# Optimization experiments

Measured on AMD Instinct MI355X. Metric: run time of the kernel, lower is better.

Reference implementation:

```python
import jax, jax.numpy as jnp
import numpy as np

N_NODES = 50000
N_EDGES = 800000
D_IN = 512
LATENT = [512, 512, 512]
L2_EPS = 1e-12  # torch F.normalize clamp_min


def _gin_layer(x, src, dst, W, b, eps):
    # sum aggregation of neighbor (source) features into destination nodes
    agg = jax.ops.segment_sum(x[src], dst, num_segments=x.shape[0])  # [N, d]
    h = agg + (1.0 + eps) * x
    return jax.nn.relu(h @ W + b)  # Sequential(Linear, ReLU)


def _l2_normalize(x):
    n = jnp.sqrt(jnp.sum(x * x, axis=-1, keepdims=True))
    return x / jnp.maximum(n, L2_EPS)


def setup_inputs() -> dict:
    key = jax.random.key(0)
    ks = jax.random.split(key, 10)
    x = jax.random.normal(ks[0], (N_NODES, D_IN), dtype=jnp.float32)
    edge_index = jax.random.randint(ks[1], (2, N_EDGES), 0, N_NODES, dtype=jnp.int32)
    dims = [D_IN] + LATENT
    inp = {"x": x, "edge_index": edge_index}
    for i in range(3):
        fan_in = dims[i]
        bound = 1.0 / np.sqrt(fan_in)
        inp[f"W{i+1}"] = jax.random.uniform(ks[2 + 2 * i], (dims[i], dims[i + 1]), jnp.float32, -bound, bound)
        inp[f"b{i+1}"] = jax.random.uniform(ks[3 + 2 * i], (dims[i + 1],), jnp.float32, -bound, bound)
        inp[f"eps{i+1}"] = jnp.zeros((), dtype=jnp.float32)  # train_eps=True, init 0
    return inp


def reference(x, edge_index, W1, b1, eps1, W2, b2, eps2, W3, b3, eps3):
    src, dst = edge_index[0], edge_index[1]
    # layers 0..num_layers-2: GINConv -> L2 normalize -> ReLU
    h = _gin_layer(x, src, dst, W1, b1, eps1)
    h = jax.nn.relu(_l2_normalize(h))
    h = _gin_layer(h, src, dst, W2, b2, eps2)
    h = jax.nn.relu(_l2_normalize(h))
    # final layer: raw GINConv output = logits
    logits = _gin_layer(h, src, dst, W3, b3, eps3)
    probs = jax.nn.softmax(logits, axis=-1)
    return (logits, probs)
```

## Files before the change

kernel.cpp:

```cpp
#include <hip/hip_runtime.h>
#include <stdint.h>

#define N_NODES 50000
#define N_EDGES 800000

typedef unsigned int uint32;

__device__ inline float bflo(uint32 u) { return __builtin_bit_cast(float, u << 16); }
__device__ inline float bfhi(uint32 u) { return __builtin_bit_cast(float, u & 0xffff0000u); }
__device__ inline float bf2f(unsigned short h) { return __builtin_bit_cast(float, (uint32)h << 16); }
__device__ inline unsigned short f2bf(float f) {
    uint32 u = __builtin_bit_cast(uint32, f);
    u += 0x7fffu + ((u >> 16) & 1u);
    return (unsigned short)(u >> 16);
}
__device__ inline uint32 pack2(float lo, float hi) {
    return (uint32)f2bf(lo) | ((uint32)f2bf(hi) << 16);
}

__global__ __launch_bounds__(256) void zero_k(int* p, int n) {
    int i = blockIdx.x * 256 + threadIdx.x;
    if (i < n) p[i] = 0;
}

__global__ __launch_bounds__(256) void count_k(const int* __restrict__ ei, int* __restrict__ cnt) {
    int e = blockIdx.x * 256 + threadIdx.x;
    if (e < N_EDGES) atomicAdd(&cnt[ei[N_EDGES + e]], 1);
}

#define NB 196

__global__ __launch_bounds__(256) void blocksum_k(const int* __restrict__ cnt, int* __restrict__ bsum) {
    int i = blockIdx.x * 256 + threadIdx.x;
    int v = (i < N_NODES) ? cnt[i] : 0;
#pragma unroll
    for (int off = 32; off > 0; off >>= 1) v += __shfl_down(v, off);
    __shared__ int sh[4];
    int w = threadIdx.x >> 6, lane = threadIdx.x & 63;
    if (lane == 0) sh[w] = v;
    __syncthreads();
    if (threadIdx.x == 0) bsum[blockIdx.x] = sh[0] + sh[1] + sh[2] + sh[3];
}

__global__ __launch_bounds__(256) void bscan_k(const int* __restrict__ bsum, int* __restrict__ bpre,
                                               int* __restrict__ rowptr) {
    __shared__ int sh[256];
    int t = threadIdx.x;
    int v = (t < NB) ? bsum[t] : 0;
    sh[t] = v;
    __syncthreads();
    for (int d = 1; d < 256; d <<= 1) {
        int u = (t >= d) ? sh[t - d] : 0;
        __syncthreads();
        sh[t] += u;
        __syncthreads();
    }
    if (t < NB) bpre[t] = sh[t] - v;
    if (t == NB - 1) rowptr[N_NODES] = sh[t];
}

__global__ __launch_bounds__(256) void scatter_k(int* __restrict__ cnt, const int* __restrict__ bpre,
                                                 int* __restrict__ rowptr) {
    int b = blockIdx.x, t = threadIdx.x, i = b * 256 + t;
    int w = t >> 6, lane = t & 63;
    int myv = (i < N_NODES) ? cnt[i] : 0;
    int v = myv;
#pragma unroll
    for (int d = 1; d < 64; d <<= 1) {
        int u = __shfl_up(v, d);
        if (lane >= d) v += u;
    }
    __shared__ int wt[4];
    if (lane == 63) wt[w] = v;
    __syncthreads();
    int off = bpre[b];
    for (int k = 0; k < w; k++) off += wt[k];
    int excl = v - myv + off;
    if (i < N_NODES) {
        rowptr[i] = excl;
        cnt[i] = excl;
    }
}

__global__ __launch_bounds__(256) void fill_k(const int* __restrict__ ei, int* __restrict__ cursor,
                                              int* __restrict__ csr) {
    int e = blockIdx.x * 256 + threadIdx.x;
    if (e < N_EDGES) {
        int d = ei[N_EDGES + e];
        int p = atomicAdd(&cursor[d], 1);
        csr[p] = ei[e];
    }
}

__global__ __launch_bounds__(256) void wprep_k(const float* __restrict__ W,
                                               unsigned short* __restrict__ Whi,
                                               unsigned short* __restrict__ Wlo) {
    __shared__ float sh[64][65];
    int bk = (blockIdx.x & 7) * 64;
    int bn = (blockIdx.x >> 3) * 64;
    int t = threadIdx.x;
    int lr = t >> 4;
    int lc4 = (t & 15) * 4;
#pragma unroll
    for (int i = 0; i < 4; i++) {
        int k = lr + i * 16;
        float4 v = *(const float4*)&W[(size_t)(bk + k) * 512 + bn + lc4];
        sh[k][lc4] = v.x; sh[k][lc4 + 1] = v.y; sh[k][lc4 + 2] = v.z; sh[k][lc4 + 3] = v.w;
    }
    __syncthreads();
#pragma unroll
    for (int i = 0; i < 4; i++) {
        int n = lr + i * 16;
        float w0 = sh[lc4][n], w1 = sh[lc4 + 1][n], w2 = sh[lc4 + 2][n], w3 = sh[lc4 + 3][n];
        ushort4 h, l;
        h.x = f2bf(w0); l.x = f2bf(w0 - bf2f(h.x));
        h.y = f2bf(w1); l.y = f2bf(w1 - bf2f(h.y));
        h.z = f2bf(w2); l.z = f2bf(w2 - bf2f(h.z));
        h.w = f2bf(w3); l.w = f2bf(w3 - bf2f(h.w));
        *(ushort4*)&Whi[(size_t)(bn + n) * 512 + bk + lc4] = h;
        *(ushort4*)&Wlo[(size_t)(bn + n) * 512 + bk + lc4] = l;
    }
}

__global__ __launch_bounds__(256) void xconv_k(const float4* __restrict__ x, uint2* __restrict__ xb) {
    int i = blockIdx.x * 256 + threadIdx.x;
    float4 v = x[i];
    uint2 o;
    o.x = pack2(v.x, v.y);
    o.y = pack2(v.z, v.w);
    xb[i] = o;
}

__global__ __launch_bounds__(256) void invn_k(const float* __restrict__ ss, float* __restrict__ invn) {
    int i = blockIdx.x * 256 + threadIdx.x;
    if (i < N_NODES) invn[i] = 1.0f / fmaxf(sqrtf(ss[i]), 1e-12f);
}

template <bool SCALED>
__global__ __launch_bounds__(256) void agg_k(const uint4* __restrict__ xin,
                                             const int* __restrict__ rowptr,
                                             const int* __restrict__ csr,
                                             const float* __restrict__ eps,
                                             const float* __restrict__ invn,
                                             uint4* __restrict__ hout) {
    int node = blockIdx.x * 4 + (threadIdx.x >> 6);
    int lane = threadIdx.x & 63;
    int beg = rowptr[node], end = rowptr[node + 1];
    float a0 = 0.f, a1 = 0.f, a2 = 0.f, a3 = 0.f, a4 = 0.f, a5 = 0.f, a6 = 0.f, a7 = 0.f;
    int e = beg;
    for (; e + 4 <= end; e += 4) {
        int s0 = csr[e], s1 = csr[e + 1], s2 = csr[e + 2], s3 = csr[e + 3];
        uint4 q0 = xin[(size_t)s0 * 64 + lane];
        uint4 q1 = xin[(size_t)s1 * 64 + lane];
        uint4 q2 = xin[(size_t)s2 * 64 + lane];
        uint4 q3 = xin[(size_t)s3 * 64 + lane];
        float w0 = SCALED ? invn[s0] : 1.0f;
        float w1 = SCALED ? invn[s1] : 1.0f;
        float w2 = SCALED ? invn[s2] : 1.0f;
        float w3 = SCALED ? invn[s3] : 1.0f;
        a0 = fmaf(w0, bflo(q0.x), fmaf(w1, bflo(q1.x), fmaf(w2, bflo(q2.x), fmaf(w3, bflo(q3.x), a0))));
        a1 = fmaf(w0, bfhi(q0.x), fmaf(w1, bfhi(q1.x), fmaf(w2, bfhi(q2.x), fmaf(w3, bfhi(q3.x), a1))));
        a2 = fmaf(w0, bflo(q0.y), fmaf(w1, bflo(q1.y), fmaf(w2, bflo(q2.y), fmaf(w3, bflo(q3.y), a2))));
        a3 = fmaf(w0, bfhi(q0.y), fmaf(w1, bfhi(q1.y), fmaf(w2, bfhi(q2.y), fmaf(w3, bfhi(q3.y), a3))));
        a4 = fmaf(w0, bflo(q0.z), fmaf(w1, bflo(q1.z), fmaf(w2, bflo(q2.z), fmaf(w3, bflo(q3.z), a4))));
        a5 = fmaf(w0, bfhi(q0.z), fmaf(w1, bfhi(q1.z), fmaf(w2, bfhi(q2.z), fmaf(w3, bfhi(q3.z), a5))));
        a6 = fmaf(w0, bflo(q0.w), fmaf(w1, bflo(q1.w), fmaf(w2, bflo(q2.w), fmaf(w3, bflo(q3.w), a6))));
        a7 = fmaf(w0, bfhi(q0.w), fmaf(w1, bfhi(q1.w), fmaf(w2, bfhi(q2.w), fmaf(w3, bfhi(q3.w), a7))));
    }
    for (; e < end; ++e) {
        int s0 = csr[e];
        uint4 q0 = xin[(size_t)s0 * 64 + lane];
        float w0 = SCALED ? invn[s0] : 1.0f;
        a0 = fmaf(w0, bflo(q0.x), a0); a1 = fmaf(w0, bfhi(q0.x), a1);
        a2 = fmaf(w0, bflo(q0.y), a2); a3 = fmaf(w0, bfhi(q0.y), a3);
        a4 = fmaf(w0, bflo(q0.z), a4); a5 = fmaf(w0, bfhi(q0.z), a5);
        a6 = fmaf(w0, bflo(q0.w), a6); a7 = fmaf(w0, bfhi(q0.w), a7);
    }
    uint4 qs = xin[(size_t)node * 64 + lane];
    float ws = (1.0f + eps[0]) * (SCALED ? invn[node] : 1.0f);
    a0 = fmaf(ws, bflo(qs.x), a0); a1 = fmaf(ws, bfhi(qs.x), a1);
    a2 = fmaf(ws, bflo(qs.y), a2); a3 = fmaf(ws, bfhi(qs.y), a3);
    a4 = fmaf(ws, bflo(qs.z), a4); a5 = fmaf(ws, bfhi(qs.z), a5);
    a6 = fmaf(ws, bflo(qs.w), a6); a7 = fmaf(ws, bfhi(qs.w), a7);
    uint4 o;
    o.x = pack2(a0, a1);
    o.y = pack2(a2, a3);
    o.z = pack2(a4, a5);
    o.w = pack2(a6, a7);
    hout[(size_t)node * 64 + lane] = o;
}

typedef __bf16 bf16x8 __attribute__((ext_vector_type(8)));
typedef float f32x4 __attribute__((ext_vector_type(4)));

__device__ inline void async16(const void* g, void* l) {
    __builtin_amdgcn_global_load_lds((const __attribute__((address_space(1))) void*)g,
                                     (__attribute__((address_space(3))) void*)l, 16, 0, 0);
}

template <bool SPLIT, bool F32OUT, bool NORM>
__global__ __launch_bounds__(256) void gemm_k(const unsigned short* __restrict__ A,
                                              const unsigned short* __restrict__ Whi,
                                              const unsigned short* __restrict__ Wlo,
                                              const float* __restrict__ bias,
                                              unsigned short* __restrict__ outB,
                                              float* __restrict__ outF,
                                              float* __restrict__ ssOut, int M) {
    constexpr int K = 512, N = 512, BK = 32, TM = 128;
    __shared__ unsigned short lds_a[TM * BK];
    __shared__ unsigned short lds_bh[TM * BK];
    __shared__ unsigned short lds_bl[SPLIT ? TM * BK : 16];
    const int t = threadIdx.x;
    const int w = t >> 6, lane = t & 63;
    const int wrow = w >> 1, wcol = w & 1;
    const int m0 = blockIdx.y * TM;
    const int n0 = blockIdx.x * TM;

    int r0 = w * 16 + (lane >> 2), cc = (lane & 3) * 8;
    int r1 = 64 + r0;
    int am0 = m0 + r0; am0 = am0 < M ? am0 : M - 1;
    int am1 = m0 + r1; am1 = am1 < M ? am1 : M - 1;
    const unsigned short* ag0 = A + (size_t)am0 * K + cc;
    const unsigned short* ag1 = A + (size_t)am1 * K + cc;
    const unsigned short* bh0 = Whi + (size_t)(n0 + r0) * K + cc;
    const unsigned short* bh1 = Whi + (size_t)(n0 + r1) * K + cc;
    const unsigned short* bl0 = Wlo + (size_t)(n0 + r0) * K + cc;
    const unsigned short* bl1 = Wlo + (size_t)(n0 + r1) * K + cc;
    unsigned short* la0 = lds_a + w * 512;
    unsigned short* la1 = lds_a + 2048 + w * 512;
    unsigned short* lh0 = lds_bh + w * 512;
    unsigned short* lh1 = lds_bh + 2048 + w * 512;
    unsigned short* ll0 = lds_bl + w * 512;
    unsigned short* ll1 = lds_bl + 2048 + w * 512;

    f32x4 acc[4][4] = {};
    const int quad = lane >> 4, l15 = lane & 15;
    const int arow = wrow * 64 + l15;
    const int brow = wcol * 64 + l15;

    for (int k0 = 0; k0 < K; k0 += BK) {
        __syncthreads();
        async16(ag0 + k0, la0);
        async16(ag1 + k0, la1);
        async16(bh0 + k0, lh0);
        async16(bh1 + k0, lh1);
        if (SPLIT) {
            async16(bl0 + k0, ll0);
            async16(bl1 + k0, ll1);
        }
        __syncthreads();
        bf16x8 af[4], bh[4], bl[4];
#pragma unroll
        for (int i = 0; i < 4; i++)
            af[i] = *(const bf16x8*)&lds_a[(arow + i * 16) * BK + quad * 8];
#pragma unroll
        for (int j = 0; j < 4; j++)
            bh[j] = *(const bf16x8*)&lds_bh[(brow + j * 16) * BK + quad * 8];
        if (SPLIT) {
#pragma unroll
            for (int j = 0; j < 4; j++)
                bl[j] = *(const bf16x8*)&lds_bl[(brow + j * 16) * BK + quad * 8];
        }
#pragma unroll
        for (int i = 0; i < 4; i++)
#pragma unroll
            for (int j = 0; j < 4; j++) {
                acc[i][j] = __builtin_amdgcn_mfma_f32_16x16x32_bf16(af[i], bh[j], acc[i][j], 0, 0, 0);
                if (SPLIT)
                    acc[i][j] = __builtin_amdgcn_mfma_f32_16x16x32_bf16(af[i], bl[j], acc[i][j], 0, 0, 0);
            }
    }

#pragma unroll
    for (int i = 0; i < 4; i++) {
        int mbase = m0 + wrow * 64 + i * 16 + quad * 4;
        float rs[4] = {0.f, 0.f, 0.f, 0.f};
#pragma unroll
        for (int j = 0; j < 4; j++) {
            int n = n0 + wcol * 64 + j * 16 + l15;
            float bv = bias[n];
#pragma unroll
            for (int r = 0; r < 4; r++) {
                int m = mbase + r;
                if (m < M) {
                    float v = fmaxf(acc[i][j][r] + bv, 0.0f);
                    if (NORM) rs[r] += v * v;
                    if (F32OUT) outF[(size_t)m * N + n] = v;
                    else        outB[(size_t)m * N + n] = f2bf(v);
                }
            }
        }
        if (NORM) {
#pragma unroll
            for (int r = 0; r < 4; r++) {
                float s = rs[r];
                s += __shfl_xor(s, 1);
                s += __shfl_xor(s, 2);
                s += __shfl_xor(s, 4);
                s += __shfl_xor(s, 8);
                int m = mbase + r;
                if (l15 == 0 && m < M) atomicAdd(&ssOut[m], s);
            }
        }
    }
}

__global__ __launch_bounds__(256) void softmax_k(const float* __restrict__ logits,
                                                 float* __restrict__ probs) {
    int node = blockIdx.x * 4 + (threadIdx.x >> 6);
    int lane = threadIdx.x & 63;
    const float4* zp = (const float4*)(logits + (size_t)node * 512);
    float4 q0 = zp[lane * 2], q1 = zp[lane * 2 + 1];
    float f[8] = {q0.x, q0.y, q0.z, q0.w, q1.x, q1.y, q1.z, q1.w};
    float m = f[0];
#pragma unroll
    for (int i = 1; i < 8; i++) m = fmaxf(m, f[i]);
#pragma unroll
    for (int off = 32; off > 0; off >>= 1) m = fmaxf(m, __shfl_xor(m, off));
    float e[8], s = 0.f;
#pragma unroll
    for (int i = 0; i < 8; i++) { e[i] = __expf(f[i] - m); s += e[i]; }
#pragma unroll
    for (int off = 32; off > 0; off >>= 1) s += __shfl_xor(s, off);
    float inv = 1.0f / s;
    float4* pp = (float4*)(probs + (size_t)node * 512);
    pp[lane * 2]     = make_float4(e[0] * inv, e[1] * inv, e[2] * inv, e[3] * inv);
    pp[lane * 2 + 1] = make_float4(e[4] * inv, e[5] * inv, e[6] * inv, e[7] * inv);
}

extern "C" void kernel_launch(void* const* d_in, const int* in_sizes, int n_in,
                              void* d_out, int out_size, void* d_ws, size_t ws_size,
                              hipStream_t stream) {
    (void)in_sizes; (void)n_in; (void)out_size; (void)ws_size;
    const float* x = (const float*)d_in[0];
    const int* ei = (const int*)d_in[1];
    const float* W1 = (const float*)d_in[2];
    const float* b1 = (const float*)d_in[3];
    const float* e1 = (const float*)d_in[4];
    const float* W2 = (const float*)d_in[5];
    const float* b2 = (const float*)d_in[6];
    const float* e2 = (const float*)d_in[7];
    const float* W3 = (const float*)d_in[8];
    const float* b3 = (const float*)d_in[9];
    const float* e3 = (const float*)d_in[10];
    float* out = (float*)d_out;
    float* out_logits = out;
    float* out_probs = out + (size_t)N_NODES * 512;

    char* ws = (char*)d_ws;
    int* rowptr = (int*)ws;
    int* cursor = rowptr + 50048;
    int* csr = cursor + 50048;
    float* invn = (float*)(csr + N_EDGES);
    int* bsum = (int*)(invn + 50048);
    int* bpre = bsum + 256;
    float* ss = (float*)(bpre + 256);
    float* ss1 = ss;
    float* ss2 = ss + 50048;
    unsigned short* Wsp = (unsigned short*)(ss + 2 * 50048);
    unsigned short* featA = Wsp + 3 * 524288;
    unsigned short* featB = featA + (size_t)N_NODES * 512;

    zero_k<<<196, 256, 0, stream>>>(cursor, N_NODES);
    zero_k<<<392, 256, 0, stream>>>((int*)ss, 2 * 50048);
    count_k<<<(N_EDGES + 255) / 256, 256, 0, stream>>>(ei, cursor);
    blocksum_k<<<NB, 256, 0, stream>>>(cursor, bsum);
    bscan_k<<<1, 256, 0, stream>>>(bsum, bpre, rowptr);
    scatter_k<<<NB, 256, 0, stream>>>(cursor, bpre, rowptr);
    fill_k<<<(N_EDGES + 255) / 256, 256, 0, stream>>>(ei, cursor, csr);

    wprep_k<<<64, 256, 0, stream>>>(W1, Wsp,           Wsp + 262144);
    wprep_k<<<64, 256, 0, stream>>>(W2, Wsp + 524288,  Wsp + 786432);
    wprep_k<<<64, 256, 0, stream>>>(W3, Wsp + 1048576, Wsp + 1310720);

    xconv_k<<<25000, 256, 0, stream>>>((const float4*)x, (uint2*)featB);

    dim3 ggrid(4, (N_NODES + 127) / 128);

    agg_k<false><<<12500, 256, 0, stream>>>((const uint4*)featB, rowptr, csr, e1, nullptr, (uint4*)featA);
    gemm_k<false, false, true><<<ggrid, 256, 0, stream>>>(featA, Wsp, Wsp + 262144, b1, featB, nullptr, ss1, N_NODES);
    invn_k<<<196, 256, 0, stream>>>(ss1, invn);
    agg_k<true><<<12500, 256, 0, stream>>>((const uint4*)featB, rowptr, csr, e2, invn, (uint4*)featA);
    gemm_k<false, false, true><<<ggrid, 256, 0, stream>>>(featA, Wsp + 524288, Wsp + 786432, b2, featB, nullptr, ss2, N_NODES);
    invn_k<<<196, 256, 0, stream>>>(ss2, invn);
    agg_k<true><<<12500, 256, 0, stream>>>((const uint4*)featB, rowptr, csr, e3, invn, (uint4*)featA);
    gemm_k<true, true, false><<<ggrid, 256, 0, stream>>>(featA, Wsp + 1048576, Wsp + 1310720, b3, nullptr, out_logits, nullptr, N_NODES);
    softmax_k<<<N_NODES / 4, 256, 0, stream>>>(out_logits, out_probs);
}
```

Measured before the change: 998.4 us.

## Fuse neighbor aggregation with GEMM, keeping aggregated tile in LDS

Merges the per-layer gather-aggregate kernel and the MFMA GEMM into one kernel: each 512-thread block aggregates 32 node rows into a swizzled LDS tile, then multiplies against weights read directly from global memory. This removes the write and re-read of the aggregated bf16 feature matrix and one launch per layer. In exchange, weight tiles are no longer staged in LDS, so each block re-reads all 512x512 weights from global/L2 with small M tiles, which lowers arithmetic reuse.

```diff
diff --git a/kernel.cpp b/kernel.cpp
--- a/kernel.cpp
+++ b/kernel.cpp
@@ -136,153 +136,127 @@
     if (i < N_NODES) invn[i] = 1.0f / fmaxf(sqrtf(ss[i]), 1e-12f);
 }
 
-template <bool SCALED>
-__global__ __launch_bounds__(256) void agg_k(const uint4* __restrict__ xin,
-                                             const int* __restrict__ rowptr,
-                                             const int* __restrict__ csr,
-                                             const float* __restrict__ eps,
-                                             const float* __restrict__ invn,
-                                             uint4* __restrict__ hout) {
-    int node = blockIdx.x * 4 + (threadIdx.x >> 6);
-    int lane = threadIdx.x & 63;
-    int beg = rowptr[node], end = rowptr[node + 1];
-    float a0 = 0.f, a1 = 0.f, a2 = 0.f, a3 = 0.f, a4 = 0.f, a5 = 0.f, a6 = 0.f, a7 = 0.f;
-    int e = beg;
-    for (; e + 4 <= end; e += 4) {
-        int s0 = csr[e], s1 = csr[e + 1], s2 = csr[e + 2], s3 = csr[e + 3];
-        uint4 q0 = xin[(size_t)s0 * 64 + lane];
-        uint4 q1 = xin[(size_t)s1 * 64 + lane];
-        uint4 q2 = xin[(size_t)s2 * 64 + lane];
-        uint4 q3 = xin[(size_t)s3 * 64 + lane];
-        float w0 = SCALED ? invn[s0] : 1.0f;
-        float w1 = SCALED ? invn[s1] : 1.0f;
-        float w2 = SCALED ? invn[s2] : 1.0f;
-        float w3 = SCALED ? invn[s3] : 1.0f;
-        a0 = fmaf(w0, bflo(q0.x), fmaf(w1, bflo(q1.x), fmaf(w2, bflo(q2.x), fmaf(w3, bflo(q3.x), a0))));
-        a1 = fmaf(w0, bfhi(q0.x), fmaf(w1, bfhi(q1.x), fmaf(w2, bfhi(q2.x), fmaf(w3, bfhi(q3.x), a1))));
-        a2 = fmaf(w0, bflo(q0.y), fmaf(w1, bflo(q1.y), fmaf(w2, bflo(q2.y), fmaf(w3, bflo(q3.y), a2))));
-        a3 = fmaf(w0, bfhi(q0.y), fmaf(w1, bfhi(q1.y), fmaf(w2, bfhi(q2.y), fmaf(w3, bfhi(q3.y), a3))));
-        a4 = fmaf(w0, bflo(q0.z), fmaf(w1, bflo(q1.z), fmaf(w2, bflo(q2.z), fmaf(w3, bflo(q3.z), a4))));
-        a5 = fmaf(w0, bfhi(q0.z), fmaf(w1, bfhi(q1.z), fmaf(w2, bfhi(q2.z), fmaf(w3, bfhi(q3.z), a5))));
-        a6 = fmaf(w0, bflo(q0.w), fmaf(w1, bflo(q1.w), fmaf(w2, bflo(q2.w), fmaf(w3, bflo(q3.w), a6))));
-        a7 = fmaf(w0, bfhi(q0.w), fmaf(w1, bfhi(q1.w), fmaf(w2, bfhi(q2.w), fmaf(w3, bfhi(q3.w), a7))));
-    }
-    for (; e < end; ++e) {
-        int s0 = csr[e];
-        uint4 q0 = xin[(size_t)s0 * 64 + lane];
-        float w0 = SCALED ? invn[s0] : 1.0f;
-        a0 = fmaf(w0, bflo(q0.x), a0); a1 = fmaf(w0, bfhi(q0.x), a1);
-        a2 = fmaf(w0, bflo(q0.y), a2); a3 = fmaf(w0, bfhi(q0.y), a3);
-        a4 = fmaf(w0, bflo(q0.z), a4); a5 = fmaf(w0, bfhi(q0.z), a5);
-        a6 = fmaf(w0, bflo(q0.w), a6); a7 = fmaf(w0, bfhi(q0.w), a7);
-    }
-    uint4 qs = xin[(size_t)node * 64 + lane];
-    float ws = (1.0f + eps[0]) * (SCALED ? invn[node] : 1.0f);
-    a0 = fmaf(ws, bflo(qs.x), a0); a1 = fmaf(ws, bfhi(qs.x), a1);
-    a2 = fmaf(ws, bflo(qs.y), a2); a3 = fmaf(ws, bfhi(qs.y), a3);
-    a4 = fmaf(ws, bflo(qs.z), a4); a5 = fmaf(ws, bfhi(qs.z), a5);
-    a6 = fmaf(ws, bflo(qs.w), a6); a7 = fmaf(ws, bfhi(qs.w), a7);
-    uint4 o;
-    o.x = pack2(a0, a1);
-    o.y = pack2(a2, a3);
-    o.z = pack2(a4, a5);
-    o.w = pack2(a6, a7);
-    hout[(size_t)node * 64 + lane] = o;
-}
-
 typedef __bf16 bf16x8 __attribute__((ext_vector_type(8)));
 typedef float f32x4 __attribute__((ext_vector_type(4)));
 
-__device__ inline void async16(const void* g, void* l) {
-    __builtin_amdgcn_global_load_lds((const __attribute__((address_space(1))) void*)g,
-                                     (__attribute__((address_space(3))) void*)l, 16, 0, 0);
-}
-
-template <bool SPLIT, bool F32OUT, bool NORM>
-__global__ __launch_bounds__(256) void gemm_k(const unsigned short* __restrict__ A,
-                                              const unsigned short* __restrict__ Whi,
-                                              const unsigned short* __restrict__ Wlo,
-                                              const float* __restrict__ bias,
-                                              unsigned short* __restrict__ outB,
-                                              float* __restrict__ outF,
-                                              float* __restrict__ ssOut, int M) {
-    constexpr int K = 512, N = 512, BK = 32, TM = 128;
-    __shared__ unsigned short lds_a[TM * BK];
-    __shared__ unsigned short lds_bh[TM * BK];
-    __shared__ unsigned short lds_bl[SPLIT ? TM * BK : 16];
+template <bool SCALED, bool SPLIT, bool F32OUT, bool NORM>
+__global__ __launch_bounds__(512, 4) void fused_k(const uint4* __restrict__ xin,
+                                                  const int* __restrict__ rowptr,
+                                                  const int* __restrict__ csr,
+                                                  const float* __restrict__ eps,
+                                                  const float* __restrict__ invn,
+                                                  const unsigned short* __restrict__ Whi,
+                                                  const unsigned short* __restrict__ Wlo,
+                                                  const float* __restrict__ bias,
+                                                  unsigned short* __restrict__ outB,
+                                                  float* __restrict__ outF,
+                                                  float* __restrict__ ssOut) {
+    constexpr int K = 512, N = 512, TM = 32;
+    __shared__ unsigned short lds_a[TM * K];
     const int t = threadIdx.x;
     const int w = t >> 6, lane = t & 63;
-    const int wrow = w >> 1, wcol = w & 1;
-    const int m0 = blockIdx.y * TM;
-    const int n0 = blockIdx.x * TM;
-
-    int r0 = w * 16 + (lane >> 2), cc = (lane & 3) * 8;
-    int r1 = 64 + r0;
-    int am0 = m0 + r0; am0 = am0 < M ? am0 : M - 1;
-    int am1 = m0 + r1; am1 = am1 < M ? am1 : M - 1;
-    const unsigned short* ag0 = A + (size_t)am0 * K + cc;
-    const unsigned short* ag1 = A + (size_t)am1 * K + cc;
-    const unsigned short* bh0 = Whi + (size_t)(n0 + r0) * K + cc;
-    const unsigned short* bh1 = Whi + (size_t)(n0 + r1) * K + cc;
-    const unsigned short* bl0 = Wlo + (size_t)(n0 + r0) * K + cc;
-    const unsigned short* bl1 = Wlo + (size_t)(n0 + r1) * K + cc;
-    unsigned short* la0 = lds_a + w * 512;
-    unsigned short* la1 = lds_a + 2048 + w * 512;
-    unsigned short* lh0 = lds_bh + w * 512;
-    unsigned short* lh1 = lds_bh + 2048 + w * 512;
-    unsigned short* ll0 = lds_bl + w * 512;
-    unsigned short* ll1 = lds_bl + 2048 + w * 512;
-
-    f32x4 acc[4][4] = {};
+    const int m0 = blockIdx.x * TM;
+
+    for (int rr = 0; rr < 4; ++rr) {
+        int row = w * 4 + rr;
+        int node = m0 + row;
+        float a0 = 0.f, a1 = 0.f, a2 = 0.f, a3 = 0.f, a4 = 0.f, a5 = 0.f, a6 = 0.f, a7 = 0.f;
+        if (node < N_NODES) {
+            int beg = rowptr[node], end = rowptr[node + 1];
+            int e = beg;
+            for (; e + 4 <= end; e += 4) {
+                int s0 = csr[e], s1 = csr[e + 1], s2 = csr[e + 2], s3 = csr[e + 3];
+                uint4 q0 = xin[(size_t)s0 * 64 + lane];
+                uint4 q1 = xin[(size_t)s1 * 64 + lane];
+                uint4 q2 = xin[(size_t)s2 * 64 + lane];
+                uint4 q3 = xin[(size_t)s3 * 64 + lane];
+                float w0 = SCALED ? invn[s0] : 1.0f;
+                float w1 = SCALED ? invn[s1] : 1.0f;
+                float w2 = SCALED ? invn[s2] : 1.0f;
+                float w3 = SCALED ? invn[s3] : 1.0f;
+                a0 = fmaf(w0, bflo(q0.x), fmaf(w1, bflo(q1.x), fmaf(w2, bflo(q2.x), fmaf(w3, bflo(q3.x), a0))));
+                a1 = fmaf(w0, bfhi(q0.x), fmaf(w1, bfhi(q1.x), fmaf(w2, bfhi(q2.x), fmaf(w3, bfhi(q3.x), a1))));
+                a2 = fmaf(w0, bflo(q0.y), fmaf(w1, bflo(q1.y), fmaf(w2, bflo(q2.y), fmaf(w3, bflo(q3.y), a2))));
+                a3 = fmaf(w0, bfhi(q0.y), fmaf(w1, bfhi(q1.y), fmaf(w2, bfhi(q2.y), fmaf(w3, bfhi(q3.y), a3))));
+                a4 = fmaf(w0, bflo(q0.z), fmaf(w1, bflo(q1.z), fmaf(w2, bflo(q2.z), fmaf(w3, bflo(q3.z), a4))));
+                a5 = fmaf(w0, bfhi(q0.z), fmaf(w1, bfhi(q1.z), fmaf(w2, bfhi(q2.z), fmaf(w3, bfhi(q3.z), a5))));
+                a6 = fmaf(w0, bflo(q0.w), fmaf(w1, bflo(q1.w), fmaf(w2, bflo(q2.w), fmaf(w3, bflo(q3.w), a6))));
+                a7 = fmaf(w0, bfhi(q0.w), fmaf(w1, bfhi(q1.w), fmaf(w2, bfhi(q2.w), fmaf(w3, bfhi(q3.w), a7))));
+            }
+            for (; e < end; ++e) {
+                int s0 = csr[e];
+                uint4 q0 = xin[(size_t)s0 * 64 + lane];
+                float w0 = SCALED ? invn[s0] : 1.0f;
+                a0 = fmaf(w0, bflo(q0.x), a0); a1 = fmaf(w0, bfhi(q0.x), a1);
+                a2 = fmaf(w0, bflo(q0.y), a2); a3 = fmaf(w0, bfhi(q0.y), a3);
+                a4 = fmaf(w0, bflo(q0.z), a4); a5 = fmaf(w0, bfhi(q0.z), a5);
+                a6 = fmaf(w0, bflo(q0.w), a6); a7 = fmaf(w0, bfhi(q0.w), a7);
+            }
+            uint4 qs = xin[(size_t)node * 64 + lane];
+            float wsf = (1.0f + eps[0]) * (SCALED ? invn[node] : 1.0f);
+            a0 = fmaf(wsf, bflo(qs.x), a0); a1 = fmaf(wsf, bfhi(qs.x), a1);
+            a2 = fmaf(wsf, bflo(qs.y), a2); a3 = fmaf(wsf, bfhi(qs.y), a3);
+            a4 = fmaf(wsf, bflo(qs.z), a4); a5 = fmaf(wsf, bfhi(qs.z), a5);
+            a6 = fmaf(wsf, bflo(qs.w), a6); a7 = fmaf(wsf, bfhi(qs.w), a7);
+        }
+        uint4 o;
+        o.x = pack2(a0, a1);
+        o.y = pack2(a2, a3);
+        o.z = pack2(a4, a5);
+        o.w = pack2(a6, a7);
+        uint32 byte = (uint32)(row * 1024 + lane * 16) ^ (uint32)((row & 7) << 4);
+        *(uint4*)((char*)lds_a + byte) = o;
+    }
+    __syncthreads();
+
     const int quad = lane >> 4, l15 = lane & 15;
-    const int arow = wrow * 64 + l15;
-    const int brow = wcol * 64 + l15;
-
-    for (int k0 = 0; k0 < K; k0 += BK) {
-        __syncthreads();
-        async16(ag0 + k0, la0);
-        async16(ag1 + k0, la1);
-        async16(bh0 + k0, lh0);
-        async16(bh1 + k0, lh1);
+    const int n0w = w * 64;
+    const uint32 swz = (uint32)((l15 & 7) << 4);
+    f32x4 acc[2][4] = {};
+    const unsigned short* bh[4];
+    const unsigned short* bl[4];
+#pragma unroll
+    for (int j = 0; j < 4; j++) {
+        bh[j] = Whi + (size_t)(n0w + j * 16 + l15) * K + quad * 8;
+        if (SPLIT) bl[j] = Wlo + (size_t)(n0w + j * 16 + l15) * K + quad * 8;
+    }
+#pragma unroll 4
+    for (int ks = 0; ks < 16; ++ks) {
+        const int k0 = ks * 32;
+        bf16x8 af[2];
+#pragma unroll
+        for (int i = 0; i < 2; i++) {
+            uint32 byte = (uint32)((i * 16 + l15) * 1024 + (k0 + quad * 8) * 2) ^ swz;
+            af[i] = *(const bf16x8*)((const char*)lds_a + byte);
+        }
+#pragma unroll
+        for (int j = 0; j < 4; j++) {
+            bf16x8 b = *(const bf16x8*)(bh[j] + k0);
+            acc[0][j] = __builtin_amdgcn_mfma_f32_16x16x32_bf16(af[0], b, acc[0][j], 0, 0, 0);
+            acc[1][j] = __builtin_amdgcn_mfma_f32_16x16x32_bf16(af[1], b, acc[1][j], 0, 0, 0);
+        }
         if (SPLIT) {
-            async16(bl0 + k0, ll0);
-            async16(bl1 + k0, ll1);
-        }
-        __syncthreads();
-        bf16x8 af[4], bh[4], bl[4];
-#pragma unroll
-        for (int i = 0; i < 4; i++)
-            af[i] = *(const bf16x8*)&lds_a[(arow + i * 16) * BK + quad * 8];
-#pragma unroll
-        for (int j = 0; j < 4; j++)
-            bh[j] = *(const bf16x8*)&lds_bh[(brow + j * 16) * BK + quad * 8];
-        if (SPLIT) {
-#pragma unroll
-            for (int j = 0; j < 4; j++)
-                bl[j] = *(const bf16x8*)&lds_bl[(brow + j * 16) * BK + quad * 8];
-        }
-#pragma unroll
-        for (int i = 0; i < 4; i++)
 #pragma unroll
             for (int j = 0; j < 4; j++) {
-                acc[i][j] = __builtin_amdgcn_mfma_f32_16x16x32_bf16(af[i], bh[j], acc[i][j], 0, 0, 0);
-                if (SPLIT)
-                    acc[i][j] = __builtin_amdgcn_mfma_f32_16x16x32_bf16(af[i], bl[j], acc[i][j], 0, 0, 0);
-            }
-    }
-
-#pragma unroll
-    for (int i = 0; i < 4; i++) {
-        int mbase = m0 + wrow * 64 + i * 16 + quad * 4;
+                bf16x8 b = *(const bf16x8*)(bl[j] + k0);
+                acc[0][j] = __builtin_amdgcn_mfma_f32_16x16x32_bf16(af[0], b, acc[0][j], 0, 0, 0);
+                acc[1][j] = __builtin_amdgcn_mfma_f32_16x16x32_bf16(af[1], b, acc[1][j], 0, 0, 0);
+            }
+        }
+    }
+
+#pragma unroll
+    for (int i = 0; i < 2; i++) {
+        int mbase = m0 + i * 16 + quad * 4;
         float rs[4] = {0.f, 0.f, 0.f, 0.f};
 #pragma unroll
         for (int j = 0; j < 4; j++) {
-            int n = n0 + wcol * 64 + j * 16 + l15;
+            int n = n0w + j * 16 + l15;
             float bv = bias[n];
 #pragma unroll
             for (int r = 0; r < 4; r++) {
                 int m = mbase + r;
-                if (m < M) {
+                if (m < N_NODES) {
                     float v = fmaxf(acc[i][j][r] + bv, 0.0f);
                     if (NORM) rs[r] += v * v;
                     if (F32OUT) outF[(size_t)m * N + n] = v;
@@ -299,7 +273,7 @@
                 s += __shfl_xor(s, 4);
                 s += __shfl_xor(s, 8);
                 int m = mbase + r;
-                if (l15 == 0 && m < M) atomicAdd(&ssOut[m], s);
+                if (l15 == 0 && m < N_NODES) atomicAdd(&ssOut[m], s);
             }
         }
     }
@@ -358,8 +332,8 @@
     float* ss1 = ss;
     float* ss2 = ss + 50048;
     unsigned short* Wsp = (unsigned short*)(ss + 2 * 50048);
-    unsigned short* featA = Wsp + 3 * 524288;
-    unsigned short* featB = featA + (size_t)N_NODES * 512;
+    unsigned short* fy = Wsp + 3 * 524288;
+    unsigned short* fx = fy + (size_t)N_NODES * 512;
 
     zero_k<<<196, 256, 0, stream>>>(cursor, N_NODES);
     zero_k<<<392, 256, 0, stream>>>((int*)ss, 2 * 50048);
@@ -373,17 +347,17 @@
     wprep_k<<<64, 256, 0, stream>>>(W2, Wsp + 524288,  Wsp + 786432);
     wprep_k<<<64, 256, 0, stream>>>(W3, Wsp + 1048576, Wsp + 1310720);
 
-    xconv_k<<<25000, 256, 0, stream>>>((const float4*)x, (uint2*)featB);
-
-    dim3 ggrid(4, (N_NODES + 127) / 128);
-
-    agg_k<false><<<12500, 256, 0, stream>>>((const uint4*)featB, rowptr, csr, e1, nullptr, (uint4*)featA);
-    gemm_k<false, false, true><<<ggrid, 256, 0, stream>>>(featA, Wsp, Wsp + 262144, b1, featB, nullptr, ss1, N_NODES);
+    xconv_k<<<25000, 256, 0, stream>>>((const float4*)x, (uint2*)fx);
+
+    const int FG = (N_NODES + 31) / 32;
+
+    fused_k<false, false, false, true><<<FG, 512, 0, stream>>>(
+        (const uint4*)fx, rowptr, csr, e1, nullptr, Wsp, nullptr, b1, fy, nullptr, ss1);
     invn_k<<<196, 256, 0, stream>>>(ss1, invn);
-    agg_k<true><<<12500, 256, 0, stream>>>((const uint4*)featB, rowptr, csr, e2, invn, (uint4*)featA);
-    gemm_k<false, false, true><<<ggrid, 256, 0, stream>>>(featA, Wsp + 524288, Wsp + 786432, b2, featB, nullptr, ss2, N_NODES);
+    fused_k<true, false, false, true><<<FG, 512, 0, stream>>>(
+        (const uint4*)fy, rowptr, csr, e2, invn, Wsp + 524288, nullptr, b2, fx, nullptr, ss2);
     invn_k<<<196, 256, 0, stream>>>(ss2, invn);
-    agg_k<true><<<12500, 256, 0, stream>>>((const uint4*)featB, rowptr, csr, e3, invn, (uint4*)featA);
-    gemm_k<true, true, false><<<ggrid, 256, 0, stream>>>(featA, Wsp + 1048576, Wsp + 1310720, b3, nullptr, out_logits, nullptr, N_NODES);
+    fused_k<true, true, true, false><<<FG, 512, 0, stream>>>(
+        (const uint4*)fx, rowptr, csr, e3, invn, Wsp + 1048576, Wsp + 1310720, b3, nullptr, out_logits, nullptr);
     softmax_k<<<N_NODES / 4, 256, 0, stream>>>(out_logits, out_probs);
 }
```

Result: slower. 1.225 ms (+22.7%).

## Pre-normalize features in a scale pass, unroll aggregation by 8, XCD-remap GEMM tiles

Applied to the files above, without the earlier changes.

Replaces the per-edge gather of inverse norms in the aggregation with a separate per-node scale kernel that writes L2-normalized bf16 features. The aggregation then does plain adds and is unrolled to eight neighbors per iteration for more loads in flight. The GEMM grid becomes 1-D and is remapped so consecutive tiles land on the same XCD for better L2 reuse. The cost is an extra full read and write of the feature matrix per layer plus a second bf16 rounding of the normalized values, and more workspace for extra buffers.

```diff
diff --git a/kernel.cpp b/kernel.cpp
--- a/kernel.cpp
+++ b/kernel.cpp
@@ -131,53 +131,63 @@
     xb[i] = o;
 }
 
-__global__ __launch_bounds__(256) void invn_k(const float* __restrict__ ss, float* __restrict__ invn) {
-    int i = blockIdx.x * 256 + threadIdx.x;
-    if (i < N_NODES) invn[i] = 1.0f / fmaxf(sqrtf(ss[i]), 1e-12f);
-}
-
-template <bool SCALED>
+__global__ __launch_bounds__(256) void scale_k(const uint4* __restrict__ in, const float* __restrict__ ss,
+                                               uint4* __restrict__ outp) {
+    int node = blockIdx.x * 4 + (threadIdx.x >> 6);
+    int lane = threadIdx.x & 63;
+    float inv = 1.0f / fmaxf(sqrtf(ss[node]), 1e-12f);
+    uint4 q = in[(size_t)node * 64 + lane];
+    uint4 o;
+    o.x = pack2(bflo(q.x) * inv, bfhi(q.x) * inv);
+    o.y = pack2(bflo(q.y) * inv, bfhi(q.y) * inv);
+    o.z = pack2(bflo(q.z) * inv, bfhi(q.z) * inv);
+    o.w = pack2(bflo(q.w) * inv, bfhi(q.w) * inv);
+    outp[(size_t)node * 64 + lane] = o;
+}
+
+#define ACC8(Q)                                                     \
+    a0 += bflo(Q.x); a1 += bfhi(Q.x); a2 += bflo(Q.y); a3 += bfhi(Q.y); \
+    a4 += bflo(Q.z); a5 += bfhi(Q.z); a6 += bflo(Q.w); a7 += bfhi(Q.w);
+
 __global__ __launch_bounds__(256) void agg_k(const uint4* __restrict__ xin,
                                              const int* __restrict__ rowptr,
                                              const int* __restrict__ csr,
                                              const float* __restrict__ eps,
-                                             const float* __restrict__ invn,
                                              uint4* __restrict__ hout) {
     int node = blockIdx.x * 4 + (threadIdx.x >> 6);
     int lane = threadIdx.x & 63;
     int beg = rowptr[node], end = rowptr[node + 1];
     float a0 = 0.f, a1 = 0.f, a2 = 0.f, a3 = 0.f, a4 = 0.f, a5 = 0.f, a6 = 0.f, a7 = 0.f;
     int e = beg;
+    for (; e + 8 <= end; e += 8) {
+        int s0 = csr[e],     s1 = csr[e + 1], s2 = csr[e + 2], s3 = csr[e + 3];
+        int s4 = csr[e + 4], s5 = csr[e + 5], s6 = csr[e + 6], s7 = csr[e + 7];
+        uint4 q0 = xin[(size_t)s0 * 64 + lane];
+        uint4 q1 = xin[(size_t)s1 * 64 + lane];
+        uint4 q2 = xin[(size_t)s2 * 64 + lane];
+        uint4 q3 = xin[(size_t)s3 * 64 + lane];
+        uint4 q4 = xin[(size_t)s4 * 64 + lane];
+        uint4 q5 = xin[(size_t)s5 * 64 + lane];
+        uint4 q6 = xin[(size_t)s6 * 64 + lane];
+        uint4 q7 = xin[(size_t)s7 * 64 + lane];
+        ACC8(q0) ACC8(q1) ACC8(q2) ACC8(q3)
+        ACC8(q4) ACC8(q5) ACC8(q6) ACC8(q7)
+    }
     for (; e + 4 <= end; e += 4) {
         int s0 = csr[e], s1 = csr[e + 1], s2 = csr[e + 2], s3 = csr[e + 3];
         uint4 q0 = xin[(size_t)s0 * 64 + lane];
         uint4 q1 = xin[(size_t)s1 * 64 + lane];
         uint4 q2 = xin[(size_t)s2 * 64 + lane];
         uint4 q3 = xin[(size_t)s3 * 64 + lane];
-        float w0 = SCALED ? invn[s0] : 1.0f;
-        float w1 = SCALED ? invn[s1] : 1.0f;
-        float w2 = SCALED ? invn[s2] : 1.0f;
-        float w3 = SCALED ? invn[s3] : 1.0f;
-        a0 = fmaf(w0, bflo(q0.x), fmaf(w1, bflo(q1.x), fmaf(w2, bflo(q2.x), fmaf(w3, bflo(q3.x), a0))));
-        a1 = fmaf(w0, bfhi(q0.x), fmaf(w1, bfhi(q1.x), fmaf(w2, bfhi(q2.x), fmaf(w3, bfhi(q3.x), a1))));
-        a2 = fmaf(w0, bflo(q0.y), fmaf(w1, bflo(q1.y), fmaf(w2, bflo(q2.y), fmaf(w3, bflo(q3.y), a2))));
-        a3 = fmaf(w0, bfhi(q0.y), fmaf(w1, bfhi(q1.y), fmaf(w2, bfhi(q2.y), fmaf(w3, bfhi(q3.y), a3))));
-        a4 = fmaf(w0, bflo(q0.z), fmaf(w1, bflo(q1.z), fmaf(w2, bflo(q2.z), fmaf(w3, bflo(q3.z), a4))));
-        a5 = fmaf(w0, bfhi(q0.z), fmaf(w1, bfhi(q1.z), fmaf(w2, bfhi(q2.z), fmaf(w3, bfhi(q3.z), a5))));
-        a6 = fmaf(w0, bflo(q0.w), fmaf(w1, bflo(q1.w), fmaf(w2, bflo(q2.w), fmaf(w3, bflo(q3.w), a6))));
-        a7 = fmaf(w0, bfhi(q0.w), fmaf(w1, bfhi(q1.w), fmaf(w2, bfhi(q2.w), fmaf(w3, bfhi(q3.w), a7))));
+        ACC8(q0) ACC8(q1) ACC8(q2) ACC8(q3)
     }
     for (; e < end; ++e) {
         int s0 = csr[e];
         uint4 q0 = xin[(size_t)s0 * 64 + lane];
-        float w0 = SCALED ? invn[s0] : 1.0f;
-        a0 = fmaf(w0, bflo(q0.x), a0); a1 = fmaf(w0, bfhi(q0.x), a1);
-        a2 = fmaf(w0, bflo(q0.y), a2); a3 = fmaf(w0, bfhi(q0.y), a3);
-        a4 = fmaf(w0, bflo(q0.z), a4); a5 = fmaf(w0, bfhi(q0.z), a5);
-        a6 = fmaf(w0, bflo(q0.w), a6); a7 = fmaf(w0, bfhi(q0.w), a7);
+        ACC8(q0)
     }
     uint4 qs = xin[(size_t)node * 64 + lane];
-    float ws = (1.0f + eps[0]) * (SCALED ? invn[node] : 1.0f);
+    float ws = 1.0f + eps[0];
     a0 = fmaf(ws, bflo(qs.x), a0); a1 = fmaf(ws, bfhi(qs.x), a1);
     a2 = fmaf(ws, bflo(qs.y), a2); a3 = fmaf(ws, bfhi(qs.y), a3);
     a4 = fmaf(ws, bflo(qs.z), a4); a5 = fmaf(ws, bfhi(qs.z), a5);
@@ -213,8 +223,13 @@
     const int t = threadIdx.x;
     const int w = t >> 6, lane = t & 63;
     const int wrow = w >> 1, wcol = w & 1;
-    const int m0 = blockIdx.y * TM;
-    const int n0 = blockIdx.x * TM;
+
+    const int nwg = gridDim.x;
+    const int qd = nwg >> 3, rd = nwg & 7;
+    const int xcd = blockIdx.x & 7, jj = blockIdx.x >> 3;
+    const int wg = (xcd < rd ? xcd * (qd + 1) : rd * (qd + 1) + (xcd - rd) * qd) + jj;
+    const int m0 = (wg >> 2) * TM;
+    const int n0 = (wg & 3) * TM;
 
     int r0 = w * 16 + (lane >> 2), cc = (lane & 3) * 8;
     int r1 = 64 + r0;
@@ -351,15 +366,16 @@
     int* rowptr = (int*)ws;
     int* cursor = rowptr + 50048;
     int* csr = cursor + 50048;
-    float* invn = (float*)(csr + N_EDGES);
-    int* bsum = (int*)(invn + 50048);
+    int* bsum = csr + N_EDGES;
     int* bpre = bsum + 256;
     float* ss = (float*)(bpre + 256);
     float* ss1 = ss;
     float* ss2 = ss + 50048;
     unsigned short* Wsp = (unsigned short*)(ss + 2 * 50048);
-    unsigned short* featA = Wsp + 3 * 524288;
-    unsigned short* featB = featA + (size_t)N_NODES * 512;
+    unsigned short* f0 = Wsp + 3 * 524288;
+    unsigned short* fA = f0 + (size_t)N_NODES * 512;
+    unsigned short* f1 = fA + (size_t)N_NODES * 512;
+    unsigned short* f2 = f1 + (size_t)N_NODES * 512;
 
     zero_k<<<196, 256, 0, stream>>>(cursor, N_NODES);
     zero_k<<<392, 256, 0, stream>>>((int*)ss, 2 * 50048);
@@ -373,17 +389,17 @@
     wprep_k<<<64, 256, 0, stream>>>(W2, Wsp + 524288,  Wsp + 786432);
     wprep_k<<<64, 256, 0, stream>>>(W3, Wsp + 1048576, Wsp + 1310720);
 
-    xconv_k<<<25000, 256, 0, stream>>>((const float4*)x, (uint2*)featB);
-
-    dim3 ggrid(4, (N_NODES + 127) / 128);
-
-    agg_k<false><<<12500, 256, 0, stream>>>((const uint4*)featB, rowptr, csr, e1, nullptr, (uint4*)featA);
-    gemm_k<false, false, true><<<ggrid, 256, 0, stream>>>(featA, Wsp, Wsp + 262144, b1, featB, nullptr, ss1, N_NODES);
-    invn_k<<<196, 256, 0, stream>>>(ss1, invn);
-    agg_k<true><<<12500, 256, 0, stream>>>((const uint4*)featB, rowptr, csr, e2, invn, (uint4*)featA);
-    gemm_k<false, false, true><<<ggrid, 256, 0, stream>>>(featA, Wsp + 524288, Wsp + 786432, b2, featB, nullptr, ss2, N_NODES);
-    invn_k<<<196, 256, 0, stream>>>(ss2, invn);
-    agg_k<true><<<12500, 256, 0, stream>>>((const uint4*)featB, rowptr, csr, e3, invn, (uint4*)featA);
-    gemm_k<true, true, false><<<ggrid, 256, 0, stream>>>(featA, Wsp + 1048576, Wsp + 1310720, b3, nullptr, out_logits, nullptr, N_NODES);
+    xconv_k<<<25000, 256, 0, stream>>>((const float4*)x, (uint2*)f0);
+
+    const int GG = 4 * ((N_NODES + 127) / 128);
+
+    agg_k<<<12500, 256, 0, stream>>>((const uint4*)f0, rowptr, csr, e1, (uint4*)fA);
+    gemm_k<false, false, true><<<GG, 256, 0, stream>>>(fA, Wsp, Wsp + 262144, b1, f1, nullptr, ss1, N_NODES);
+    scale_k<<<12500, 256, 0, stream>>>((const uint4*)f1, ss1, (uint4*)f2);
+    agg_k<<<12500, 256, 0, stream>>>((const uint4*)f2, rowptr, csr, e2, (uint4*)fA);
+    gemm_k<false, false, true><<<GG, 256, 0, stream>>>(fA, Wsp + 524288, Wsp + 786432, b2, f1, nullptr, ss2, N_NODES);
+    scale_k<<<12500, 256, 0, stream>>>((const uint4*)f1, ss2, (uint4*)f2);
+    agg_k<<<12500, 256, 0, stream>>>((const uint4*)f2, rowptr, csr, e3, (uint4*)fA);
+    gemm_k<true, true, false><<<GG, 256, 0, stream>>>(fA, Wsp + 1048576, Wsp + 1310720, b3, nullptr, out_logits, nullptr, N_NODES);
     softmax_k<<<N_NODES / 4, 256, 0, stream>>>(out_logits, out_probs);
 }
```

Result: no change. 1.004 ms (+0.5%).
